# Optimization experiments

Measured on AMD Instinct MI355X. Metric: run time of the kernel, lower is better.

Reference implementation:

```python
import jax, jax.numpy as jnp
import numpy as np

B, S, E, H = 2, 2048, 1024, 16  # batch, max_seq_length, embedding_dim, num_heads
D = E // H  # head dim = 64


def setup_inputs() -> dict:
    key = jax.random.key(0)
    ks = jax.random.split(key, 7)
    scale = 0.02
    return {
        "inputs": jax.random.normal(ks[0], (B, S, E), jnp.float32),
        "embbeding_V": jax.random.normal(ks[1], (B, S, E), jnp.float32),
        "embbeding_K": jax.random.normal(ks[2], (B, S, E), jnp.float32),
        "Wq": jax.random.normal(ks[3], (E, E), jnp.float32) * scale,
        "Wk": jax.random.normal(ks[4], (E, E), jnp.float32) * scale,
        "Wv": jax.random.normal(ks[5], (E, E), jnp.float32) * scale,
        "Wo": jax.random.normal(ks[6], (E, E), jnp.float32) * scale,
    }


def reference(inputs, embbeding_V, embbeding_K, Wq, Wk, Wv, Wo):
    b = inputs.shape[0]
    # repeat last token of `inputs` to max_seq_length: [b, S, E]
    x = jnp.broadcast_to(inputs[:, -1, :][:, None, :], (b, S, E))
    # torch Linear(bias=False): y = x @ W.T ; split heads -> [b, H, S, D]
    q = (x @ Wq.T).reshape(b, S, H, D).transpose(0, 2, 1, 3)
    k = (embbeding_K @ Wk.T).reshape(b, S, H, D).transpose(0, 2, 1, 3)
    v = (embbeding_V @ Wv.T).reshape(b, S, H, D).transpose(0, 2, 1, 3)
    # UNSCALED attention (faithful to source: no 1/sqrt(d))
    s = jnp.einsum("bhqd,bhkd->bhqk", q, k)
    p = jax.nn.softmax(s, axis=-1)
    o = jnp.einsum("bhqk,bhkd->bhqd", p, v)
    # transpose(1,2) then reshape to [b, S, E]
    o = o.transpose(0, 2, 1, 3).reshape(b, S, E)
    return o @ Wo.T
```

## Files before the change

### kernel.cpp

```cpp
#include <hip/hip_runtime.h>
#include <hip/hip_bf16.h>

constexpr int B = 2, S = 2048, E = 1024, H = 16, D = 64;
constexpr int E4 = E / 4;

__global__ void k_qvec(const float4* __restrict__ x, const float4* __restrict__ Wq,
                       float* __restrict__ q_vec) {
  int blk = blockIdx.x;
  int b = blk >> 7, n0 = (blk & 127) * 8;
  int tid = threadIdx.x;
  int nl = tid >> 5, es = tid & 31;
  const float4* xr = x + ((size_t)b * S + (S - 1)) * E4;
  const float4* wr = Wq + (size_t)(n0 + nl) * E4;
  float acc = 0.f;
#pragma unroll
  for (int j = 0; j < 8; ++j) {
    float4 a = xr[es + 32 * j];
    float4 w = wr[es + 32 * j];
    acc += a.x * w.x + a.y * w.y + a.z * w.z + a.w * w.w;
  }
#pragma unroll
  for (int o = 16; o > 0; o >>= 1) acc += __shfl_xor(acc, o, 64);
  if (es == 0) q_vec[b * E + n0 + nl] = acc;
}

__global__ void k_wkq(const float* __restrict__ q_vec, const float* __restrict__ Wk,
                      float* __restrict__ wkq, float* __restrict__ rowsum) {
  int blk = blockIdx.x;
  int eo = blk & 7;
  int bh = blk >> 3;
  int h = bh & 15;
  int tid = threadIdx.x;
  __shared__ float qh[D];
  if (tid < D) qh[tid] = q_vec[(bh >> 4) * E + h * D + tid];
  if (eo == 0 && tid == 0) rowsum[bh] = 0.f;
  __syncthreads();
  int e = eo * 128 + tid;
  const float* wp = Wk + (size_t)h * D * E + e;
  float acc = 0.f;
#pragma unroll 8
  for (int d = 0; d < D; ++d) acc += qh[d] * wp[(size_t)d * E];
  wkq[(size_t)bh * E + e] = acc;
}

__global__ __launch_bounds__(128) void k_scores_exp(const float4* __restrict__ embK,
                                                    const float4* __restrict__ wkq4,
                                                    float* __restrict__ p,
                                                    float* __restrict__ rowsum) {
  __shared__ float4 wl[H * E4];
  __shared__ float hsum[16];
  int blk = blockIdx.x;
  int b = blk >> 7, k0 = (blk & 127) * 16;
  int tid = threadIdx.x;
#pragma unroll
  for (int j = 0; j < 32; ++j)
    wl[j * 128 + tid] = wkq4[(size_t)b * (H * E4) + j * 128 + tid];
  if (tid < 16) hsum[tid] = 0.f;
  __syncthreads();
  int kp = tid >> 4, es = tid & 15;
  int ka = k0 + kp, kb = k0 + 8 + kp;
  const float4* ea = embK + ((size_t)b * S + ka) * E4;
  const float4* eb = embK + ((size_t)b * S + kb) * E4;
  float4 va[16], vb[16];
#pragma unroll
  for (int j = 0; j < 16; ++j) { va[j] = ea[es + 16 * j]; vb[j] = eb[es + 16 * j]; }
#pragma unroll 1
  for (int h = 0; h < H; ++h) {
    float aa = 0.f, ab = 0.f;
#pragma unroll
    for (int j = 0; j < 16; ++j) {
      float4 w = wl[h * 256 + es + 16 * j];
      aa += va[j].x * w.x + va[j].y * w.y + va[j].z * w.z + va[j].w * w.w;
      ab += vb[j].x * w.x + vb[j].y * w.y + vb[j].z * w.z + vb[j].w * w.w;
    }
#pragma unroll
    for (int o = 8; o > 0; o >>= 1) {
      aa += __shfl_xor(aa, o, 64);
      ab += __shfl_xor(ab, o, 64);
    }
    if (es == 0) {
      float pa = __expf(aa), pb = __expf(ab);
      float* pr = p + ((size_t)(b * H + h)) * S;
      pr[ka] = pa;
      pr[kb] = pb;
      atomicAdd(&hsum[h], pa + pb);
    }
  }
  __syncthreads();
  if (tid < 16) atomicAdd(&rowsum[b * H + tid], hsum[tid]);
}

__global__ __launch_bounds__(256) void k_ctx_part(const float4* __restrict__ embV,
                                                  const float* __restrict__ p,
                                                  const float* __restrict__ rowsum,
                                                  float4* __restrict__ part) {
  int b = blockIdx.x, eo = blockIdx.y, kz = blockIdx.z;
  int tid = threadIdx.x;
  int e4l = tid & 63, w = tid >> 6;
  int k0 = kz * 128;
  __shared__ float pl[16 * 128];
  __shared__ float sinv[16];
  if (tid < 16) sinv[tid] = 1.f / rowsum[b * H + tid];
  __syncthreads();
  for (int i = tid; i < 16 * 128; i += 256) {
    int h = i >> 7, kk = i & 127;
    pl[i] = p[((size_t)(b * H + h)) * S + k0 + kk] * sinv[h];
  }
  __syncthreads();
  int e4 = eo * 64 + e4l;
  float4 acc[H];
#pragma unroll
  for (int h = 0; h < H; ++h) acc[h] = make_float4(0.f, 0.f, 0.f, 0.f);
  int kb = w * 32;
  for (int i = 0; i < 32; ++i) {
    int kk = kb + i;
    float4 v = embV[((size_t)b * S + k0 + kk) * E4 + e4];
#pragma unroll
    for (int h = 0; h < H; ++h) {
      float pv = pl[h * 128 + kk];
      acc[h].x += pv * v.x; acc[h].y += pv * v.y;
      acc[h].z += pv * v.z; acc[h].w += pv * v.w;
    }
  }
  int pz = kz * 4 + w;
#pragma unroll
  for (int h = 0; h < H; ++h)
    part[((size_t)(pz * B + b) * H + h) * E4 + e4] = acc[h];
}

__global__ __launch_bounds__(256) void k_ovec(const float4* __restrict__ part,
                                              const float4* __restrict__ Wv4,
                                              float* __restrict__ o_vec) {
  int b = blockIdx.x, h = blockIdx.y;
  int t = threadIdx.x;
  __shared__ float4 crow[E4];
  float4 acc = make_float4(0.f, 0.f, 0.f, 0.f);
  const float4* pp = part + ((size_t)b * H + h) * E4 + t;
  const size_t pstride = (size_t)B * H * E4;
#pragma unroll 8
  for (int pz = 0; pz < 64; ++pz) {
    float4 c = pp[pz * pstride];
    acc.x += c.x; acc.y += c.y; acc.z += c.z; acc.w += c.w;
  }
  crow[t] = acc;
  __syncthreads();
  int n_l = t >> 2, p4 = t & 3;
  const float4* wr = Wv4 + (size_t)(h * 64 + n_l) * E4 + p4 * 64;
  float a = 0.f;
#pragma unroll 8
  for (int j = 0; j < 64; ++j) {
    float4 c = crow[p4 * 64 + j];
    float4 w = wr[j];
    a += c.x * w.x + c.y * w.y + c.z * w.z + c.w * w.w;
  }
  a += __shfl_xor(a, 1, 64);
  a += __shfl_xor(a, 2, 64);
  if (p4 == 0) o_vec[(size_t)b * E + h * 64 + n_l] = a;
}

__global__ void k_outvec(const float* __restrict__ o_vec, const float4* __restrict__ Wo4,
                         float* __restrict__ out_vec) {
  int gw = (blockIdx.x * blockDim.x + threadIdx.x) >> 6;
  int lane = threadIdx.x & 63;
  int b = gw >> 10, nn = gw & 1023;
  const float4* xr = (const float4*)(o_vec + (size_t)b * E);
  const float4* wr = Wo4 + (size_t)nn * E4;
  float acc = 0.f;
#pragma unroll
  for (int j = 0; j < 4; ++j) {
    float4 a = xr[lane + 64 * j];
    float4 w = wr[lane + 64 * j];
    acc += a.x * w.x + a.y * w.y + a.z * w.z + a.w * w.w;
  }
#pragma unroll
  for (int o = 32; o > 0; o >>= 1) acc += __shfl_xor(acc, o, 64);
  if (lane == 0) out_vec[gw] = acc;
}

__global__ void k_bcast(const float4* __restrict__ ov4, float4* __restrict__ out4) {
  int base = blockIdx.x * 1024 + threadIdx.x;
#pragma unroll
  for (int r = 0; r < 4; ++r) {
    int g = base + r * 256;
    out4[g] = ov4[(g >> 19) * E4 + (g & 255)];
  }
}

extern "C" void kernel_launch(void* const* d_in, const int* in_sizes, int n_in,
                              void* d_out, int out_size, void* d_ws, size_t ws_size,
                              hipStream_t stream) {
  const float* inputs = (const float*)d_in[0];
  const float* embV   = (const float*)d_in[1];
  const float* embK   = (const float*)d_in[2];
  const float* Wq     = (const float*)d_in[3];
  const float* Wk     = (const float*)d_in[4];
  const float* Wv     = (const float*)d_in[5];
  const float* Wo     = (const float*)d_in[6];

  float* ws      = (float*)d_ws;
  float* q_vec   = ws;
  float* wkq     = q_vec + B * E;
  float* p       = wkq + B * H * E;
  float* rowsum  = p + B * H * S;
  float* o_vec   = rowsum + 64;
  float* out_vec = o_vec + B * E;
  float* part    = out_vec + B * E;

  k_qvec<<<256, 256, 0, stream>>>((const float4*)inputs, (const float4*)Wq, q_vec);
  k_wkq<<<256, 128, 0, stream>>>(q_vec, Wk, wkq, rowsum);
  k_scores_exp<<<256, 128, 0, stream>>>((const float4*)embK, (const float4*)wkq,
                                        p, rowsum);
  k_ctx_part<<<dim3(B, 4, 16), 256, 0, stream>>>((const float4*)embV, p, rowsum,
                                                 (float4*)part);
  k_ovec<<<dim3(B, H), 256, 0, stream>>>((const float4*)part, (const float4*)Wv, o_vec);
  k_outvec<<<512, 256, 0, stream>>>(o_vec, (const float4*)Wo, out_vec);
  k_bcast<<<1024, 256, 0, stream>>>((const float4*)out_vec, (float4*)d_out);
}
```

Measured before the change: 156.7 us.

## Widen ctx partial grid and split Wv projection into reduce plus wave-per-row kernels

k_ctx_part now runs twice as many blocks, each covering half as many e4 columns, with two k-subgroups per wave merged by a cross-half shuffle. The old k_ovec used only 32 blocks to both reduce 64 partials and apply Wv. It is replaced by k_reduce (256 blocks that sum the partials into a ctx buffer) and k_ovec_wave (one wave per output row of Wv). The aim is more parallelism in the tail stages, at the cost of one more kernel launch and an extra ctx round trip through global memory.

```diff
diff --git a/kernel.cpp b/kernel.cpp
--- a/kernel.cpp
+++ b/kernel.cpp
@@ -96,7 +96,7 @@
                                                   float4* __restrict__ part) {
   int b = blockIdx.x, eo = blockIdx.y, kz = blockIdx.z;
   int tid = threadIdx.x;
-  int e4l = tid & 63, w = tid >> 6;
+  int e4l = tid & 31, ksub = tid >> 5;
   int k0 = kz * 128;
   __shared__ float pl[16 * 128];
   __shared__ float sinv[16];
@@ -107,12 +107,12 @@
     pl[i] = p[((size_t)(b * H + h)) * S + k0 + kk] * sinv[h];
   }
   __syncthreads();
-  int e4 = eo * 64 + e4l;
+  int e4 = eo * 32 + e4l;
   float4 acc[H];
 #pragma unroll
   for (int h = 0; h < H; ++h) acc[h] = make_float4(0.f, 0.f, 0.f, 0.f);
-  int kb = w * 32;
-  for (int i = 0; i < 32; ++i) {
+  int kb = ksub * 16;
+  for (int i = 0; i < 16; ++i) {
     int kk = kb + i;
     float4 v = embV[((size_t)b * S + k0 + kk) * E4 + e4];
 #pragma unroll
@@ -122,40 +122,63 @@
       acc[h].z += pv * v.z; acc[h].w += pv * v.w;
     }
   }
-  int pz = kz * 4 + w;
-#pragma unroll
-  for (int h = 0; h < H; ++h)
-    part[((size_t)(pz * B + b) * H + h) * E4 + e4] = acc[h];
-}
-
-__global__ __launch_bounds__(256) void k_ovec(const float4* __restrict__ part,
-                                              const float4* __restrict__ Wv4,
-                                              float* __restrict__ o_vec) {
-  int b = blockIdx.x, h = blockIdx.y;
-  int t = threadIdx.x;
-  __shared__ float4 crow[E4];
+#pragma unroll
+  for (int h = 0; h < H; ++h) {
+    acc[h].x += __shfl_xor(acc[h].x, 32, 64);
+    acc[h].y += __shfl_xor(acc[h].y, 32, 64);
+    acc[h].z += __shfl_xor(acc[h].z, 32, 64);
+    acc[h].w += __shfl_xor(acc[h].w, 32, 64);
+  }
+  if ((tid & 63) < 32) {
+    int pz = kz * 4 + (tid >> 6);
+#pragma unroll
+    for (int h = 0; h < H; ++h)
+      part[((size_t)(pz * B + b) * H + h) * E4 + e4] = acc[h];
+  }
+}
+
+__global__ __launch_bounds__(128) void k_reduce(const float4* __restrict__ part,
+                                                float4* __restrict__ ctx4) {
+  int b = blockIdx.x, h = blockIdx.y, eo = blockIdx.z;
+  int tid = threadIdx.x;
+  int e4l = tid & 31, psub = tid >> 5;
+  int e4 = eo * 32 + e4l;
+  const size_t pstride = (size_t)B * H * E4;
+  const float4* pp = part + ((size_t)b * H + h) * E4 + e4 + psub * 16 * pstride;
   float4 acc = make_float4(0.f, 0.f, 0.f, 0.f);
-  const float4* pp = part + ((size_t)b * H + h) * E4 + t;
-  const size_t pstride = (size_t)B * H * E4;
-#pragma unroll 8
-  for (int pz = 0; pz < 64; ++pz) {
-    float4 c = pp[pz * pstride];
+#pragma unroll
+  for (int j = 0; j < 16; ++j) {
+    float4 c = pp[j * pstride];
     acc.x += c.x; acc.y += c.y; acc.z += c.z; acc.w += c.w;
   }
-  crow[t] = acc;
-  __syncthreads();
-  int n_l = t >> 2, p4 = t & 3;
-  const float4* wr = Wv4 + (size_t)(h * 64 + n_l) * E4 + p4 * 64;
-  float a = 0.f;
-#pragma unroll 8
-  for (int j = 0; j < 64; ++j) {
-    float4 c = crow[p4 * 64 + j];
-    float4 w = wr[j];
-    a += c.x * w.x + c.y * w.y + c.z * w.z + c.w * w.w;
-  }
-  a += __shfl_xor(a, 1, 64);
-  a += __shfl_xor(a, 2, 64);
-  if (p4 == 0) o_vec[(size_t)b * E + h * 64 + n_l] = a;
+  __shared__ float4 red[128];
+  red[tid] = acc;
+  __syncthreads();
+  if (tid < 32) {
+    float4 a0 = red[tid], a1 = red[tid + 32], a2 = red[tid + 64], a3 = red[tid + 96];
+    float4 r = make_float4(a0.x + a1.x + a2.x + a3.x, a0.y + a1.y + a2.y + a3.y,
+                           a0.z + a1.z + a2.z + a3.z, a0.w + a1.w + a2.w + a3.w);
+    ctx4[((size_t)b * H + h) * E4 + e4] = r;
+  }
+}
+
+__global__ void k_ovec_wave(const float* __restrict__ ctx, const float4* __restrict__ Wv4,
+                            float* __restrict__ o_vec) {
+  int gw = (blockIdx.x * blockDim.x + threadIdx.x) >> 6;
+  int lane = threadIdx.x & 63;
+  int b = gw >> 10, nn = gw & 1023;
+  const float4* xr = (const float4*)(ctx + ((size_t)(b * H + (nn >> 6))) * E);
+  const float4* wr = Wv4 + (size_t)nn * E4;
+  float acc = 0.f;
+#pragma unroll
+  for (int j = 0; j < 4; ++j) {
+    float4 a = xr[lane + 64 * j];
+    float4 w = wr[lane + 64 * j];
+    acc += a.x * w.x + a.y * w.y + a.z * w.z + a.w * w.w;
+  }
+#pragma unroll
+  for (int o = 32; o > 0; o >>= 1) acc += __shfl_xor(acc, o, 64);
+  if (lane == 0) o_vec[gw] = acc;
 }
 
 __global__ void k_outvec(const float* __restrict__ o_vec, const float4* __restrict__ Wo4,
@@ -205,14 +228,16 @@
   float* o_vec   = rowsum + 64;
   float* out_vec = o_vec + B * E;
   float* part    = out_vec + B * E;
+  float* ctx     = part + 64 * B * H * E;
 
   k_qvec<<<256, 256, 0, stream>>>((const float4*)inputs, (const float4*)Wq, q_vec);
   k_wkq<<<256, 128, 0, stream>>>(q_vec, Wk, wkq, rowsum);
   k_scores_exp<<<256, 128, 0, stream>>>((const float4*)embK, (const float4*)wkq,
                                         p, rowsum);
-  k_ctx_part<<<dim3(B, 4, 16), 256, 0, stream>>>((const float4*)embV, p, rowsum,
+  k_ctx_part<<<dim3(B, 8, 16), 256, 0, stream>>>((const float4*)embV, p, rowsum,
                                                  (float4*)part);
-  k_ovec<<<dim3(B, H), 256, 0, stream>>>((const float4*)part, (const float4*)Wv, o_vec);
+  k_reduce<<<dim3(B, H, 8), 128, 0, stream>>>((const float4*)part, (float4*)ctx);
+  k_ovec_wave<<<512, 256, 0, stream>>>(ctx, (const float4*)Wv, o_vec);
   k_outvec<<<512, 256, 0, stream>>>(o_vec, (const float4*)Wo, out_vec);
   k_bcast<<<1024, 256, 0, stream>>>((const float4*)out_vec, (float4*)d_out);
 }
```

After: 148.4 us. 5.3% less time.
